# Kernel tuning notes

Measured on AMD Instinct MI355X. Metric: run time of the kernel, lower is better.

Reference implementation:

```python
import jax, jax.numpy as jnp
import numpy as np

H = 2048      # hidden_size
L = 350       # max_length

def setup_inputs() -> dict:
    key = jax.random.key(0)
    ks = jax.random.split(key, 12)
    s = 0.02
    return {
        "input": jax.random.normal(ks[0], (1, 1, H), jnp.float32),
        "hidden": jax.random.normal(ks[1], (1, 1, H), jnp.float32),
        "encoder_outputs": jax.random.normal(ks[2], (L, H), jnp.float32),
        # nn.Linear(2H, L)
        "attn_W": jax.random.normal(ks[3], (L, 2 * H), jnp.float32) * s,
        "attn_b": jax.random.normal(ks[4], (L,), jnp.float32) * s,
        # nn.Linear(2H, H)
        "comb_W": jax.random.normal(ks[5], (H, 2 * H), jnp.float32) * s,
        "comb_b": jax.random.normal(ks[6], (H,), jnp.float32) * s,
        # nn.GRU(H, H) single layer weights (PyTorch layout: [3H, H])
        "w_ih": jax.random.normal(ks[7], (3 * H, H), jnp.float32) * s,
        "w_hh": jax.random.normal(ks[8], (3 * H, H), jnp.float32) * s,
        "b_ih": jax.random.normal(ks[9], (3 * H,), jnp.float32) * s,
        "b_hh": jax.random.normal(ks[10], (3 * H,), jnp.float32) * s,
    }

def reference(input, hidden, encoder_outputs, attn_W, attn_b, comb_W, comb_b, w_ih, w_hh, b_ih, b_hh):
    x = input.reshape(1, H)          # (1, H)  == reshape(input,(1,1,H))[0]
    h = hidden[0]                    # (1, H)
    # Bahdanau-style attention over fixed max_length slots
    attn_weights = jax.nn.softmax(jnp.concatenate([x, h], axis=1) @ attn_W.T + attn_b, axis=1)  # (1, L)
    context = attn_weights @ encoder_outputs                                                    # (1, H)
    # combine + relu (dropout is defined but never applied in the original forward)
    g = jax.nn.relu(jnp.concatenate([x, context], axis=1) @ comb_W.T + comb_b)                  # (1, H)
    # single GRU step (PyTorch gate order: reset, update, new)
    gi = g @ w_ih.T + b_ih           # (1, 3H)
    gh = h @ w_hh.T + b_hh           # (1, 3H)
    i_r, i_z, i_n = jnp.split(gi, 3, axis=1)
    h_r, h_z, h_n = jnp.split(gh, 3, axis=1)
    r = jax.nn.sigmoid(i_r + h_r)
    z = jax.nn.sigmoid(i_z + h_z)
    n = jnp.tanh(i_n + r * h_n)
    h_new = (1.0 - z) * n + z * h    # (1, H)
    output = h_new[None]             # (1, 1, H)
    return (output, h_new[None], attn_weights)
```

## Files before the change

### kernel.cpp

```cpp
#include <hip/hip_runtime.h>
#include <math.h>

#define H 2048
#define L 350

__device__ __forceinline__ float dot4(float4 a, float4 b, float acc) {
    acc = fmaf(a.x, b.x, acc);
    acc = fmaf(a.y, b.y, acc);
    acc = fmaf(a.z, b.z, acc);
    acc = fmaf(a.w, b.w, acc);
    return acc;
}

__device__ __forceinline__ float wsum(float v) {
    #pragma unroll
    for (int m = 1; m < 64; m <<= 1) v += __shfl_xor(v, m, 64);
    return v;
}
__device__ __forceinline__ float wmax(float v) {
    #pragma unroll
    for (int m = 1; m < 64; m <<= 1) v = fmaxf(v, __shfl_xor(v, m, 64));
    return v;
}

__global__ __launch_bounds__(256) void k1_logits_gh(
    const float* __restrict__ input, const float* __restrict__ hidden,
    const float* __restrict__ attn_W, const float* __restrict__ attn_b,
    const float* __restrict__ w_hh, const float* __restrict__ b_hh,
    float* __restrict__ logits, float* __restrict__ gh)
{
    const int w = threadIdx.x >> 6, lane = threadIdx.x & 63;
    const int item = blockIdx.x * 4 + w;
    const float4* x4 = reinterpret_cast<const float4*>(input);
    const float4* h4 = reinterpret_cast<const float4*>(hidden);
    if (item < L) {
        const float4* Wr = reinterpret_cast<const float4*>(attn_W + (size_t)item * (2 * H));
        float acc = 0.f;
        #pragma unroll
        for (int i = lane; i < H / 4; i += 64) {
            acc = dot4(Wr[i], x4[i], acc);
            acc = dot4(Wr[H / 4 + i], h4[i], acc);
        }
        acc = wsum(acc);
        if (lane == 0) logits[item] = acc + attn_b[item];
    } else if (item < L + 3 * H) {
        const int row = item - L;
        const float4* Wr = reinterpret_cast<const float4*>(w_hh + (size_t)row * H);
        float acc = 0.f;
        #pragma unroll
        for (int i = lane; i < H / 4; i += 64) acc = dot4(Wr[i], h4[i], acc);
        acc = wsum(acc);
        if (lane == 0) gh[row] = acc + b_hh[row];
    }
}

__global__ __launch_bounds__(256) void k2_softmax_ctx(
    const float* __restrict__ logits, const float* __restrict__ enc,
    float* __restrict__ ctx, float* __restrict__ attn_out)
{
    __shared__ float attn_s[L];
    __shared__ float smax[4], ssum[4];
    __shared__ float partial[8][32];
    const int t = threadIdx.x, w = t >> 6, lane = t & 63;

    float v0 = (t < L) ? logits[t] : -INFINITY;
    float v1 = (t + 256 < L) ? logits[t + 256] : -INFINITY;
    float m = wmax(fmaxf(v0, v1));
    if (lane == 0) smax[w] = m;
    __syncthreads();
    m = fmaxf(fmaxf(smax[0], smax[1]), fmaxf(smax[2], smax[3]));
    float e0 = (t < L) ? expf(v0 - m) : 0.f;
    float e1 = (t + 256 < L) ? expf(v1 - m) : 0.f;
    float s = wsum(e0 + e1);
    if (lane == 0) ssum[w] = s;
    __syncthreads();
    const float inv = 1.f / (ssum[0] + ssum[1] + ssum[2] + ssum[3]);
    if (t < L) attn_s[t] = e0 * inv;
    if (t + 256 < L) attn_s[t + 256] = e1 * inv;
    if (blockIdx.x == 0) {
        if (t < L) attn_out[t] = e0 * inv;
        if (t + 256 < L) attn_out[t + 256] = e1 * inv;
    }
    __syncthreads();

    const int col_l = t & 31, k = t >> 5;
    const int col = blockIdx.x * 32 + col_l;
    const float* ec = enc + col;
    float a0 = 0.f, a1 = 0.f, a2 = 0.f, a3 = 0.f;
    int j = k;
    for (; j + 24 < L; j += 32) {
        a0 = fmaf(attn_s[j],      ec[(size_t)j * H],        a0);
        a1 = fmaf(attn_s[j + 8],  ec[(size_t)(j + 8) * H],  a1);
        a2 = fmaf(attn_s[j + 16], ec[(size_t)(j + 16) * H], a2);
        a3 = fmaf(attn_s[j + 24], ec[(size_t)(j + 24) * H], a3);
    }
    for (; j < L; j += 8) a0 = fmaf(attn_s[j], ec[(size_t)j * H], a0);
    partial[k][col_l] = (a0 + a1) + (a2 + a3);
    __syncthreads();
    if (t < 32) {
        float acc = 0.f;
        #pragma unroll
        for (int kk = 0; kk < 8; ++kk) acc += partial[kk][t];
        ctx[blockIdx.x * 32 + t] = acc;
    }
}

__global__ __launch_bounds__(256) void k3_combine(
    const float* __restrict__ input, const float* __restrict__ ctx,
    const float* __restrict__ comb_W, const float* __restrict__ comb_b,
    float* __restrict__ g)
{
    const int w = threadIdx.x >> 6, lane = threadIdx.x & 63;
    const int r = blockIdx.x * 4 + w;
    const float4* x4 = reinterpret_cast<const float4*>(input);
    const float4* c4 = reinterpret_cast<const float4*>(ctx);
    const float4* Wr = reinterpret_cast<const float4*>(comb_W + (size_t)r * (2 * H));
    float acc = 0.f;
    #pragma unroll
    for (int i = lane; i < H / 4; i += 64) {
        acc = dot4(Wr[i], x4[i], acc);
        acc = dot4(Wr[H / 4 + i], c4[i], acc);
    }
    acc = wsum(acc);
    if (lane == 0) g[r] = fmaxf(acc + comb_b[r], 0.f);
}

__global__ __launch_bounds__(256) void k4_gru(
    const float* __restrict__ g, const float* __restrict__ hidden,
    const float* __restrict__ w_ih, const float* __restrict__ b_ih,
    const float* __restrict__ gh, float* __restrict__ out)
{
    const int w = threadIdx.x >> 6, lane = threadIdx.x & 63;
    const int item = blockIdx.x * 4 + w;
    const float4* g4 = reinterpret_cast<const float4*>(g);
    const float4* Wr0 = reinterpret_cast<const float4*>(w_ih + (size_t)item * H);
    const float4* Wr1 = reinterpret_cast<const float4*>(w_ih + (size_t)(item + H) * H);
    const float4* Wr2 = reinterpret_cast<const float4*>(w_ih + (size_t)(item + 2 * H) * H);
    float ar = 0.f, az = 0.f, an = 0.f;
    #pragma unroll
    for (int i = lane; i < H / 4; i += 64) {
        const float4 gv = g4[i];
        ar = dot4(Wr0[i], gv, ar);
        az = dot4(Wr1[i], gv, az);
        an = dot4(Wr2[i], gv, an);
    }
    ar = wsum(ar); az = wsum(az); an = wsum(an);
    if (lane == 0) {
        const float ir  = ar + b_ih[item];
        const float iz  = az + b_ih[item + H];
        const float in_ = an + b_ih[item + 2 * H];
        const float r = 1.f / (1.f + expf(-(ir + gh[item])));
        const float z = 1.f / (1.f + expf(-(iz + gh[item + H])));
        const float n = tanhf(in_ + r * gh[item + 2 * H]);
        const float hnew = (1.f - z) * n + z * hidden[item];
        out[item] = hnew;
        out[H + item] = hnew;
    }
}

extern "C" void kernel_launch(void* const* d_in, const int* in_sizes, int n_in,
                              void* d_out, int out_size, void* d_ws, size_t ws_size,
                              hipStream_t stream)
{
    const float* input  = (const float*)d_in[0];
    const float* hidden = (const float*)d_in[1];
    const float* enc    = (const float*)d_in[2];
    const float* attn_W = (const float*)d_in[3];
    const float* attn_b = (const float*)d_in[4];
    const float* comb_W = (const float*)d_in[5];
    const float* comb_b = (const float*)d_in[6];
    const float* w_ih   = (const float*)d_in[7];
    const float* w_hh   = (const float*)d_in[8];
    const float* b_ih   = (const float*)d_in[9];
    const float* b_hh   = (const float*)d_in[10];
    float* out = (float*)d_out;
    float* ws  = (float*)d_ws;

    float* logits = ws;
    float* gh     = ws + 512;
    float* g      = ws + 7168;
    float* ctx    = ws + 9216;

    k1_logits_gh<<<(L + 3 * H + 3) / 4, 256, 0, stream>>>(
        input, hidden, attn_W, attn_b, w_hh, b_hh, logits, gh);
    k2_softmax_ctx<<<64, 256, 0, stream>>>(logits, enc, ctx, out + 2 * H);
    k3_combine<<<H / 4, 256, 0, stream>>>(input, ctx, comb_W, comb_b, g);
    k4_gru<<<H / 4, 256, 0, stream>>>(g, hidden, w_ih, b_ih, gh, out);
}
```

Measured before the change: 38.43 us.

## Fuse decoder stages into one persistent kernel with atomic work queues

Replaces the four kernel launches with a single persistent kernel of 512 blocks that claims work through global atomic counters and waits on completion counters between dependent stages. The w_hh GEMV work is spread across the gaps where blocks wait for the logits and context stages, so it overlaps them. ctx and g are staged into shared memory per block. This removes inter-kernel launch gaps and tail effects. In exchange it adds atomic traffic, a memset launch, and spin-waits that depend on all 512 blocks being co-resident.

```diff
diff --git a/kernel.cpp b/kernel.cpp
--- a/kernel.cpp
+++ b/kernel.cpp
@@ -3,6 +3,34 @@
 
 #define H 2048
 #define L 350
+#define NB 512
+
+#define OFF_GH   512
+#define OFF_G    7168
+#define OFF_CTX  9216
+#define OFF_CNT  12288
+
+#define W_LOG 0
+#define D_LOG 1
+#define W_GH  2
+#define D_GH  3
+#define W_CTX 4
+#define D_CTX 5
+#define W_CMB 6
+#define D_CMB 7
+#define W_GRU 8
+
+#define VMCNT0() asm volatile("s_waitcnt vmcnt(0)" ::: "memory")
+
+__device__ __forceinline__ float cload(const float* p) {
+    return __hip_atomic_load(p, __ATOMIC_RELAXED, __HIP_MEMORY_SCOPE_AGENT);
+}
+__device__ __forceinline__ void cstore(float* p, float v) {
+    __hip_atomic_store(p, v, __ATOMIC_RELAXED, __HIP_MEMORY_SCOPE_AGENT);
+}
+__device__ __forceinline__ unsigned iadd(unsigned* p, unsigned v) {
+    return __hip_atomic_fetch_add(p, v, __ATOMIC_RELAXED, __HIP_MEMORY_SCOPE_AGENT);
+}
 
 __device__ __forceinline__ float dot4(float4 a, float4 b, float acc) {
     acc = fmaf(a.x, b.x, acc);
@@ -11,7 +39,6 @@
     acc = fmaf(a.w, b.w, acc);
     return acc;
 }
-
 __device__ __forceinline__ float wsum(float v) {
     #pragma unroll
     for (int m = 1; m < 64; m <<= 1) v += __shfl_xor(v, m, 64);
@@ -23,138 +50,238 @@
     return v;
 }
 
-__global__ __launch_bounds__(256) void k1_logits_gh(
+__global__ __launch_bounds__(256, 2) void fused_decoder(
     const float* __restrict__ input, const float* __restrict__ hidden,
+    const float* __restrict__ enc,
     const float* __restrict__ attn_W, const float* __restrict__ attn_b,
-    const float* __restrict__ w_hh, const float* __restrict__ b_hh,
-    float* __restrict__ logits, float* __restrict__ gh)
+    const float* __restrict__ comb_W, const float* __restrict__ comb_b,
+    const float* __restrict__ w_ih, const float* __restrict__ w_hh,
+    const float* __restrict__ b_ih, const float* __restrict__ b_hh,
+    float* __restrict__ out, float* __restrict__ ws)
 {
-    const int w = threadIdx.x >> 6, lane = threadIdx.x & 63;
-    const int item = blockIdx.x * 4 + w;
+    __shared__ __align__(16) float sh[2048];
+    __shared__ float smax[4], ssum[4];
+    __shared__ float part[8][32];
+    __shared__ unsigned claim_s, done_s;
+
+    float* logits = ws;
+    float* gh     = ws + OFF_GH;
+    float* g      = ws + OFF_G;
+    float* ctx    = ws + OFF_CTX;
+    unsigned* cnt = (unsigned*)(ws + OFF_CNT);
+
+    const int tid = threadIdx.x, wv = tid >> 6, lane = tid & 63;
     const float4* x4 = reinterpret_cast<const float4*>(input);
     const float4* h4 = reinterpret_cast<const float4*>(hidden);
-    if (item < L) {
-        const float4* Wr = reinterpret_cast<const float4*>(attn_W + (size_t)item * (2 * H));
-        float acc = 0.f;
-        #pragma unroll
-        for (int i = lane; i < H / 4; i += 64) {
-            acc = dot4(Wr[i], x4[i], acc);
-            acc = dot4(Wr[H / 4 + i], h4[i], acc);
-        }
-        acc = wsum(acc);
-        if (lane == 0) logits[item] = acc + attn_b[item];
-    } else if (item < L + 3 * H) {
-        const int row = item - L;
-        const float4* Wr = reinterpret_cast<const float4*>(w_hh + (size_t)row * H);
-        float acc = 0.f;
-        #pragma unroll
-        for (int i = lane; i < H / 4; i += 64) acc = dot4(Wr[i], h4[i], acc);
-        acc = wsum(acc);
-        if (lane == 0) gh[row] = acc + b_hh[row];
-    }
-}
-
-__global__ __launch_bounds__(256) void k2_softmax_ctx(
-    const float* __restrict__ logits, const float* __restrict__ enc,
-    float* __restrict__ ctx, float* __restrict__ attn_out)
-{
-    __shared__ float attn_s[L];
-    __shared__ float smax[4], ssum[4];
-    __shared__ float partial[8][32];
-    const int t = threadIdx.x, w = t >> 6, lane = t & 63;
-
-    float v0 = (t < L) ? logits[t] : -INFINITY;
-    float v1 = (t + 256 < L) ? logits[t + 256] : -INFINITY;
-    float m = wmax(fmaxf(v0, v1));
-    if (lane == 0) smax[w] = m;
+
+    for (;;) {
+        __syncthreads();
+        if (tid == 0) claim_s = iadd(&cnt[W_LOG], 4);
+        __syncthreads();
+        const unsigned r0 = claim_s;
+        if (r0 >= L) break;
+        const unsigned r = r0 + wv;
+        if (r < L) {
+            const float4* Wr = reinterpret_cast<const float4*>(attn_W + (size_t)r * (2 * H));
+            float acc = 0.f;
+            #pragma unroll
+            for (int i = lane; i < H / 4; i += 64) {
+                acc = dot4(Wr[i], x4[i], acc);
+                acc = dot4(Wr[H / 4 + i], h4[i], acc);
+            }
+            acc = wsum(acc);
+            if (lane == 0) cstore(&logits[r], acc + attn_b[r]);
+        }
+        VMCNT0();
+        __syncthreads();
+        if (tid == 0) iadd(&cnt[D_LOG], 4);
+    }
+
+    for (;;) {
+        __syncthreads();
+        if (tid == 0) {
+            done_s = (iadd(&cnt[D_LOG], 0) >= 352u) ? 1u : 0u;
+            claim_s = done_s ? 0xFFFFFFFFu : iadd(&cnt[W_GH], 16);
+        }
+        __syncthreads();
+        if (done_s) break;
+        const unsigned base = claim_s;
+        if (base < 3 * H) {
+            const unsigned r0 = base + wv * 4;
+            for (unsigned r = r0; r < r0 + 4; ++r) {
+                const float4* Wr = reinterpret_cast<const float4*>(w_hh + (size_t)r * H);
+                float acc = 0.f;
+                #pragma unroll
+                for (int i = lane; i < H / 4; i += 64) acc = dot4(Wr[i], h4[i], acc);
+                acc = wsum(acc);
+                if (lane == 0) cstore(&gh[r], acc + b_hh[r]);
+            }
+            VMCNT0();
+            __syncthreads();
+            if (tid == 0) iadd(&cnt[D_GH], 16);
+        } else {
+            if (tid == 0) __builtin_amdgcn_s_sleep(4);
+        }
+    }
+
+    {
+        float v0 = (tid < L) ? cload(&logits[tid]) : -INFINITY;
+        float v1 = (tid + 256 < L) ? cload(&logits[tid + 256]) : -INFINITY;
+        float m = wmax(fmaxf(v0, v1));
+        if (lane == 0) smax[wv] = m;
+        __syncthreads();
+        m = fmaxf(fmaxf(smax[0], smax[1]), fmaxf(smax[2], smax[3]));
+        float e0 = (tid < L) ? expf(v0 - m) : 0.f;
+        float e1 = (tid + 256 < L) ? expf(v1 - m) : 0.f;
+        float s = wsum(e0 + e1);
+        if (lane == 0) ssum[wv] = s;
+        __syncthreads();
+        const float inv = 1.f / (ssum[0] + ssum[1] + ssum[2] + ssum[3]);
+        if (tid < L) sh[tid] = e0 * inv;
+        if (tid + 256 < L) sh[tid + 256] = e1 * inv;
+        __syncthreads();
+    }
+
+    for (;;) {
+        __syncthreads();
+        if (tid == 0) claim_s = iadd(&cnt[W_CTX], 1);
+        __syncthreads();
+        const unsigned item = claim_s;
+        if (item >= 64) break;
+        if (item == 0) {
+            if (tid < L) out[2 * H + tid] = sh[tid];
+            if (tid + 256 < L) out[2 * H + tid + 256] = sh[tid + 256];
+        }
+        const int col_l = tid & 31, k = tid >> 5;
+        const int col = item * 32 + col_l;
+        const float* ec = enc + col;
+        float a0 = 0.f, a1 = 0.f, a2 = 0.f, a3 = 0.f;
+        int j = k;
+        for (; j + 24 < L; j += 32) {
+            a0 = fmaf(sh[j],      ec[(size_t)j * H],        a0);
+            a1 = fmaf(sh[j + 8],  ec[(size_t)(j + 8) * H],  a1);
+            a2 = fmaf(sh[j + 16], ec[(size_t)(j + 16) * H], a2);
+            a3 = fmaf(sh[j + 24], ec[(size_t)(j + 24) * H], a3);
+        }
+        for (; j < L; j += 8) a0 = fmaf(sh[j], ec[(size_t)j * H], a0);
+        part[k][col_l] = (a0 + a1) + (a2 + a3);
+        __syncthreads();
+        if (tid < 32) {
+            float acc = 0.f;
+            #pragma unroll
+            for (int kk = 0; kk < 8; ++kk) acc += part[kk][tid];
+            cstore(&ctx[item * 32 + tid], acc);
+        }
+        VMCNT0();
+        __syncthreads();
+        if (tid == 0) iadd(&cnt[D_CTX], 1);
+    }
+
+    for (;;) {
+        __syncthreads();
+        if (tid == 0) claim_s = iadd(&cnt[W_GH], 16);
+        __syncthreads();
+        const unsigned base = claim_s;
+        if (base >= 3 * H) break;
+        const unsigned r0 = base + wv * 4;
+        for (unsigned r = r0; r < r0 + 4; ++r) {
+            const float4* Wr = reinterpret_cast<const float4*>(w_hh + (size_t)r * H);
+            float acc = 0.f;
+            #pragma unroll
+            for (int i = lane; i < H / 4; i += 64) acc = dot4(Wr[i], h4[i], acc);
+            acc = wsum(acc);
+            if (lane == 0) cstore(&gh[r], acc + b_hh[r]);
+        }
+        VMCNT0();
+        __syncthreads();
+        if (tid == 0) iadd(&cnt[D_GH], 16);
+    }
+
+    if (tid == 0) {
+        for (int it = 0; it < (1 << 24); ++it) {
+            if (iadd(&cnt[D_CTX], 0) >= 64u) break;
+            __builtin_amdgcn_s_sleep(4);
+        }
+    }
     __syncthreads();
-    m = fmaxf(fmaxf(smax[0], smax[1]), fmaxf(smax[2], smax[3]));
-    float e0 = (t < L) ? expf(v0 - m) : 0.f;
-    float e1 = (t + 256 < L) ? expf(v1 - m) : 0.f;
-    float s = wsum(e0 + e1);
-    if (lane == 0) ssum[w] = s;
+    for (int i = tid; i < H; i += 256) sh[i] = cload(&ctx[i]);
     __syncthreads();
-    const float inv = 1.f / (ssum[0] + ssum[1] + ssum[2] + ssum[3]);
-    if (t < L) attn_s[t] = e0 * inv;
-    if (t + 256 < L) attn_s[t + 256] = e1 * inv;
-    if (blockIdx.x == 0) {
-        if (t < L) attn_out[t] = e0 * inv;
-        if (t + 256 < L) attn_out[t + 256] = e1 * inv;
+
+    {
+        const float4* c4 = reinterpret_cast<const float4*>(sh);
+        for (;;) {
+            __syncthreads();
+            if (tid == 0) claim_s = iadd(&cnt[W_CMB], 8);
+            __syncthreads();
+            const unsigned base = claim_s;
+            if (base >= H) break;
+            const unsigned r0 = base + wv * 2;
+            for (unsigned r = r0; r < r0 + 2; ++r) {
+                const float4* Wr = reinterpret_cast<const float4*>(comb_W + (size_t)r * (2 * H));
+                float acc = 0.f;
+                #pragma unroll
+                for (int i = lane; i < H / 4; i += 64) {
+                    acc = dot4(Wr[i], x4[i], acc);
+                    acc = dot4(Wr[H / 4 + i], c4[i], acc);
+                }
+                acc = wsum(acc);
+                if (lane == 0) cstore(&g[r], fmaxf(acc + comb_b[r], 0.f));
+            }
+            VMCNT0();
+            __syncthreads();
+            if (tid == 0) iadd(&cnt[D_CMB], 8);
+        }
+    }
+
+    if (tid == 0) {
+        for (int it = 0; it < (1 << 24); ++it) {
+            if (iadd(&cnt[D_CMB], 0) >= (unsigned)H &&
+                iadd(&cnt[D_GH], 0) >= (unsigned)(3 * H)) break;
+            __builtin_amdgcn_s_sleep(4);
+        }
     }
     __syncthreads();
-
-    const int col_l = t & 31, k = t >> 5;
-    const int col = blockIdx.x * 32 + col_l;
-    const float* ec = enc + col;
-    float a0 = 0.f, a1 = 0.f, a2 = 0.f, a3 = 0.f;
-    int j = k;
-    for (; j + 24 < L; j += 32) {
-        a0 = fmaf(attn_s[j],      ec[(size_t)j * H],        a0);
-        a1 = fmaf(attn_s[j + 8],  ec[(size_t)(j + 8) * H],  a1);
-        a2 = fmaf(attn_s[j + 16], ec[(size_t)(j + 16) * H], a2);
-        a3 = fmaf(attn_s[j + 24], ec[(size_t)(j + 24) * H], a3);
-    }
-    for (; j < L; j += 8) a0 = fmaf(attn_s[j], ec[(size_t)j * H], a0);
-    partial[k][col_l] = (a0 + a1) + (a2 + a3);
+    for (int i = tid; i < H; i += 256) sh[i] = cload(&g[i]);
     __syncthreads();
-    if (t < 32) {
-        float acc = 0.f;
-        #pragma unroll
-        for (int kk = 0; kk < 8; ++kk) acc += partial[kk][t];
-        ctx[blockIdx.x * 32 + t] = acc;
-    }
-}
-
-__global__ __launch_bounds__(256) void k3_combine(
-    const float* __restrict__ input, const float* __restrict__ ctx,
-    const float* __restrict__ comb_W, const float* __restrict__ comb_b,
-    float* __restrict__ g)
-{
-    const int w = threadIdx.x >> 6, lane = threadIdx.x & 63;
-    const int r = blockIdx.x * 4 + w;
-    const float4* x4 = reinterpret_cast<const float4*>(input);
-    const float4* c4 = reinterpret_cast<const float4*>(ctx);
-    const float4* Wr = reinterpret_cast<const float4*>(comb_W + (size_t)r * (2 * H));
-    float acc = 0.f;
-    #pragma unroll
-    for (int i = lane; i < H / 4; i += 64) {
-        acc = dot4(Wr[i], x4[i], acc);
-        acc = dot4(Wr[H / 4 + i], c4[i], acc);
-    }
-    acc = wsum(acc);
-    if (lane == 0) g[r] = fmaxf(acc + comb_b[r], 0.f);
-}
-
-__global__ __launch_bounds__(256) void k4_gru(
-    const float* __restrict__ g, const float* __restrict__ hidden,
-    const float* __restrict__ w_ih, const float* __restrict__ b_ih,
-    const float* __restrict__ gh, float* __restrict__ out)
-{
-    const int w = threadIdx.x >> 6, lane = threadIdx.x & 63;
-    const int item = blockIdx.x * 4 + w;
-    const float4* g4 = reinterpret_cast<const float4*>(g);
-    const float4* Wr0 = reinterpret_cast<const float4*>(w_ih + (size_t)item * H);
-    const float4* Wr1 = reinterpret_cast<const float4*>(w_ih + (size_t)(item + H) * H);
-    const float4* Wr2 = reinterpret_cast<const float4*>(w_ih + (size_t)(item + 2 * H) * H);
-    float ar = 0.f, az = 0.f, an = 0.f;
-    #pragma unroll
-    for (int i = lane; i < H / 4; i += 64) {
-        const float4 gv = g4[i];
-        ar = dot4(Wr0[i], gv, ar);
-        az = dot4(Wr1[i], gv, az);
-        an = dot4(Wr2[i], gv, an);
-    }
-    ar = wsum(ar); az = wsum(az); an = wsum(an);
-    if (lane == 0) {
-        const float ir  = ar + b_ih[item];
-        const float iz  = az + b_ih[item + H];
-        const float in_ = an + b_ih[item + 2 * H];
-        const float r = 1.f / (1.f + expf(-(ir + gh[item])));
-        const float z = 1.f / (1.f + expf(-(iz + gh[item + H])));
-        const float n = tanhf(in_ + r * gh[item + 2 * H]);
-        const float hnew = (1.f - z) * n + z * hidden[item];
-        out[item] = hnew;
-        out[H + item] = hnew;
+
+    {
+        const float4* g4 = reinterpret_cast<const float4*>(sh);
+        for (;;) {
+            __syncthreads();
+            if (tid == 0) claim_s = iadd(&cnt[W_GRU], 8);
+            __syncthreads();
+            const unsigned base = claim_s;
+            if (base >= H) break;
+            const unsigned c0 = base + wv * 2;
+            for (unsigned col = c0; col < c0 + 2; ++col) {
+                const float4* Wr0 = reinterpret_cast<const float4*>(w_ih + (size_t)col * H);
+                const float4* Wr1 = reinterpret_cast<const float4*>(w_ih + (size_t)(col + H) * H);
+                const float4* Wr2 = reinterpret_cast<const float4*>(w_ih + (size_t)(col + 2 * H) * H);
+                float ar = 0.f, az = 0.f, an = 0.f;
+                #pragma unroll
+                for (int i = lane; i < H / 4; i += 64) {
+                    const float4 gv = g4[i];
+                    ar = dot4(Wr0[i], gv, ar);
+                    az = dot4(Wr1[i], gv, az);
+                    an = dot4(Wr2[i], gv, an);
+                }
+                ar = wsum(ar); az = wsum(az); an = wsum(an);
+                if (lane == 0) {
+                    const float ir  = ar + b_ih[col];
+                    const float iz  = az + b_ih[col + H];
+                    const float in_ = an + b_ih[col + 2 * H];
+                    const float hr = cload(&gh[col]);
+                    const float hz = cload(&gh[col + H]);
+                    const float hn = cload(&gh[col + 2 * H]);
+                    const float r = 1.f / (1.f + expf(-(ir + hr)));
+                    const float z = 1.f / (1.f + expf(-(iz + hz)));
+                    const float n = tanhf(in_ + r * hn);
+                    const float hnew = (1.f - z) * n + z * hidden[col];
+                    out[col] = hnew;
+                    out[H + col] = hnew;
+                }
+            }
+        }
     }
 }
 
@@ -176,14 +303,9 @@
     float* out = (float*)d_out;
     float* ws  = (float*)d_ws;
 
-    float* logits = ws;
-    float* gh     = ws + 512;
-    float* g      = ws + 7168;
-    float* ctx    = ws + 9216;
-
-    k1_logits_gh<<<(L + 3 * H + 3) / 4, 256, 0, stream>>>(
-        input, hidden, attn_W, attn_b, w_hh, b_hh, logits, gh);
-    k2_softmax_ctx<<<64, 256, 0, stream>>>(logits, enc, ctx, out + 2 * H);
-    k3_combine<<<H / 4, 256, 0, stream>>>(input, ctx, comb_W, comb_b, g);
-    k4_gru<<<H / 4, 256, 0, stream>>>(g, hidden, w_ih, b_ih, gh, out);
-}
+    hipMemsetAsync(ws + OFF_CNT, 0, 64, stream);
+
+    fused_decoder<<<NB, 256, 0, stream>>>(
+        input, hidden, enc, attn_W, attn_b, comb_W, comb_b,
+        w_ih, w_hh, b_ih, b_hh, out, ws);
+}
```

New measurement: 137.4 us. +257.6%, slower.
